# Optimization experiments

Measured on AMD Instinct MI355X. Metric: run time of the kernel, lower is better.

The kernel has to match this reference:

```python
import jax, jax.numpy as jnp
import numpy as np

BETA = 0.9       # neuron_args['beta']
THRESH = 0.5     # neuron_args['threshold'] (mem_thresh)
ALPHA = 2.0      # surrogate.atan(alpha=2)
BIN = 50         # int(0.2 / 0.004)
NSTEPS = 7       # num_steps
STEP = BIN // NSTEPS  # 7 -> only buffer[:49] is used


@jax.custom_vjp
def atan_spike(x):
    return (x > 0).astype(x.dtype)

def _asp_fwd(x):
    return (x > 0).astype(x.dtype), x

def _asp_bwd(x, g):
    return (g * (ALPHA / 2.0) / (1.0 + (jnp.pi / 2.0 * ALPHA * x) ** 2),)

atan_spike.defvjp(_asp_fwd, _asp_bwd)


def _heaviside_detached(x):
    # snntorch mem_reset: reset = spike_grad(mem - thresh).detach()
    return jax.lax.stop_gradient((x > 0).astype(x.dtype))


def _forward(x, W_in, W_h0, W_out, v_x, v_y):
    T, B, D = x.shape
    H = W_in.shape[0]
    O = W_out.shape[0]
    vxy = jnp.concatenate([v_x, v_y])  # (2,)

    def single_forward(acc):  # acc: (NSTEPS, B, D)
        mem1 = jnp.zeros((B, H), x.dtype)
        mem2 = jnp.zeros((B, H), x.dtype)
        mem_out = jnp.zeros((B, O), x.dtype)
        for s in range(NSTEPS):
            cur = acc[s] @ W_in.T                      # (B, H); dropout in eval mode = identity
            reset = _heaviside_detached(mem1 - THRESH)
            mem1 = (BETA * mem1 + cur) * (1.0 - reset)  # reset_mechanism='zero'
            spk = atan_spike(mem1 - THRESH)
            cur = spk @ W_h0.T
            reset = _heaviside_detached(mem2 - THRESH)
            mem2 = (BETA * mem2 + cur) * (1.0 - reset)
            spk = atan_spike(mem2 - THRESH)
            cur = spk @ W_out.T                        # (B, O)
            mem_out = BETA * mem_out + cur             # reset_mechanism='none'
        return mem_out

    def step(carry, x_t):
        buf, L = carry  # buf: (BIN, B, D) zero-padded past L valid frames
        # torch: append then trim front when >BIN. While growing, frames keep
        # fixed positions with zeros at the end (NOT a sliding window yet).
        grow = jax.lax.dynamic_update_slice_in_dim(buf, x_t[None], L, 0)
        slide = jnp.concatenate([buf[1:], x_t[None]], axis=0)
        buf = jnp.where(L < BIN, grow, slide)
        L = jnp.minimum(L + 1, BIN)
        # acc_spikes[i] = sum(buf[7i : 7i+7]); frame 49 unused (49 = 7*7)
        acc = buf[: NSTEPS * STEP].reshape(NSTEPS, STEP, B, D).sum(axis=1)
        pred = single_forward(acc)                     # (B, 2)
        return (buf, L), pred * vxy

    init = (jnp.zeros((BIN, B, D), x.dtype), jnp.int32(1))  # one initial zero frame
    _, preds = jax.lax.scan(step, init, x)             # (T, B, 2)
    return preds


def setup_inputs() -> dict:
    key = jax.random.key(0)
    ks = jax.random.split(key, 6)
    T, B, D, H, O = 128, 1024, 96, 128, 2
    x = jax.random.uniform(ks[0], (T, B, D), dtype=jnp.float32)
    W_in = jax.random.normal(ks[1], (H, D), dtype=jnp.float32) / np.sqrt(D)
    W_h0 = jax.random.normal(ks[2], (H, H), dtype=jnp.float32) / np.sqrt(H)
    W_out = jax.random.normal(ks[3], (O, H), dtype=jnp.float32) / np.sqrt(H)
    v_x = jax.random.normal(ks[4], (1,), dtype=jnp.float32)
    v_y = jax.random.normal(ks[5], (1,), dtype=jnp.float32)
    return {"x": x, "W_in": W_in, "W_h0": W_h0, "W_out": W_out, "v_x": v_x, "v_y": v_y}


def reference(x, W_in, W_h0, W_out, v_x, v_y):
    return _forward(x, W_in, W_h0, W_out, v_x, v_y)
```

## Files before the change

kernel.cpp:

```cpp
#include <hip/hip_runtime.h>
#include <cstdint>

#define T_STEPS 128
#define BATCH   1024
#define D_INPUT 96
#define H_DIM   128
#define NWIN    163

__device__ __forceinline__ void win_decode(int widx, int& start, int& len) {
    if (widx < 121)      { start = widx;        len = 7; }
    else if (widx < 127) { start = 0;           len = widx - 120; }
    else { const int r = widx - 127; const int s = 1 + r / 6;
           len = 1 + r % 6;          start = 7 * s - 1; }
}

__device__ __forceinline__ int widx_for(int t, int s) {
    if (t >= 49) return t - 49 + 7 * s;
    if (s == 0)  return 121 + min(5, t);
    const int st = 7 * s - 1;
    if (t < st) return -1;
    const int len = min(7, t - st + 1);
    return (len == 7) ? st : (127 + (s - 1) * 6 + (len - 1));
}

__device__ __forceinline__ int swz_idx(int row, int col) {
    return (row << 7) | (col ^ ((row & 63) << 1));
}

__global__ __launch_bounds__(256) void kA_wincur(const float* __restrict__ x,
                                                 const float* __restrict__ Win,
                                                 float* __restrict__ CUR1) {
    __shared__ float xs[D_INPUT * 32];
    __shared__ float wT[D_INPUT * H_DIM];
    const int widx = blockIdx.x;
    const int b0   = blockIdx.y * 32;
    int start, len; win_decode(widx, start, len);
    const int tid = threadIdx.x;

    for (int e = tid; e < H_DIM * D_INPUT; e += 256) {
        const int h = e / D_INPUT, d = e % D_INPUT;
        wT[swz_idx(d, h)] = Win[e];
    }
    for (int e = tid; e < D_INPUT * 32; e += 256) {
        const int d = e % D_INPUT, bq = e / D_INPUT;
        const float* xp = x + ((size_t)start * BATCH + b0 + bq) * D_INPUT + d;
        float s = xp[0];
        for (int k = 1; k < len; ++k)
            s = __fadd_rn(s, xp[(size_t)k * BATCH * D_INPUT]);
        xs[d * 32 + bq] = s;
    }
    __syncthreads();

    const int hp = tid & 63, g = tid >> 6;
    const int h0 = hp << 1;
    float acc[8][2];
#pragma unroll
    for (int r = 0; r < 8; ++r) { acc[r][0] = 0.f; acc[r][1] = 0.f; }

#pragma unroll 6
    for (int d = 0; d < D_INPUT; ++d) {
        const float2 wp  = *(const float2*)&wT[swz_idx(d, h0)];
        const float4 xv0 = *(const float4*)&xs[d * 32 + g * 8];
        const float4 xv1 = *(const float4*)&xs[d * 32 + g * 8 + 4];
        const float xv[8] = {xv0.x,xv0.y,xv0.z,xv0.w, xv1.x,xv1.y,xv1.z,xv1.w};
#pragma unroll
        for (int r = 0; r < 8; ++r) {
            acc[r][0] = __fmaf_rn(xv[r], wp.x, acc[r][0]);
            acc[r][1] = __fmaf_rn(xv[r], wp.y, acc[r][1]);
        }
    }
    float* op = CUR1 + ((size_t)widx * BATCH + b0 + g * 8) * H_DIM + h0;
#pragma unroll
    for (int r = 0; r < 8; ++r) {
        float2 o; o.x = acc[r][0]; o.y = acc[r][1];
        *(float2*)(op + (size_t)r * H_DIM) = o;
    }
}

__global__ __launch_bounds__(512, 2) void kB_snn(const float* __restrict__ CUR1,
                                                 const float* __restrict__ Wh0,
                                                 const float* __restrict__ Wout,
                                                 const float* __restrict__ vxp,
                                                 const float* __restrict__ vyp,
                                                 float* __restrict__ out) {
    __shared__ float lw[H_DIM * H_DIM];
    __shared__ float sf[8][64 * 32];
    const int tid = threadIdx.x;
    for (int e = tid; e < H_DIM * H_DIM; e += 512) {
        const int i = e >> 7, h = e & 127;
        lw[swz_idx(h, i)] = Wh0[e];
    }
    __syncthreads();

    const int w = tid >> 6, lane = tid & 63;
    const int t  = blockIdx.y;
    const int i0 = lane << 1;
    float* sfw = sf[w];
    const int lbase = lane * 32;
    const float wex = Wout[i0],     wey = Wout[H_DIM + i0];
    const float wox = Wout[i0 + 1], woy = Wout[H_DIM + i0 + 1];
    const float vx = vxp[0], vy = vyp[0];
    const int b0 = (blockIdx.x << 7) + (w << 4);

    float m1a[16], m1b[16], m2a[16], m2b[16], poa[16], pob[16];
    float c1a[16], c1b[16];
    bool  s1a[16], s1b[16], s2a[16], s2b[16];
#pragma unroll
    for (int k = 0; k < 16; ++k) {
        m1a[k]=0.f; m1b[k]=0.f; m2a[k]=0.f; m2b[k]=0.f; poa[k]=0.f; pob[k]=0.f;
        s1a[k]=false; s1b[k]=false; s2a[k]=false; s2b[k]=false;
    }

    {
        const int wi = widx_for(t, 0);
#pragma unroll
        for (int k = 0; k < 16; ++k) {
            c1a[k] = 0.f; c1b[k] = 0.f;
            if (wi >= 0) {
                const float2 v = *(const float2*)
                    &CUR1[((size_t)wi * BATCH + b0 + k) * H_DIM + i0];
                c1a[k] = v.x; c1b[k] = v.y;
            }
        }
    }

#pragma unroll 1
    for (int s = 0; s < 7; ++s) {
        float sev[16], sov[16];
#pragma unroll
        for (int k = 0; k < 16; ++k) {
            m1a[k] = s1a[k] ? 0.f : __fadd_rn(__fmul_rn(0.9f, m1a[k]), c1a[k]);
            m1b[k] = s1b[k] ? 0.f : __fadd_rn(__fmul_rn(0.9f, m1b[k]), c1b[k]);
            s1a[k] = m1a[k] > 0.5f; s1b[k] = m1b[k] > 0.5f;
            sev[k] = s1a[k] ? 1.0f : 0.0f;
            sov[k] = s1b[k] ? 1.0f : 0.0f;
        }
#pragma unroll
        for (int c = 0; c < 4; ++c) {
            float4 v;
            v.x = sev[c*4]; v.y = sev[c*4+1]; v.z = sev[c*4+2]; v.w = sev[c*4+3];
            *(float4*)&sfw[lbase + ((c     ^ (lane & 7)) << 2)] = v;
            v.x = sov[c*4]; v.y = sov[c*4+1]; v.z = sov[c*4+2]; v.w = sov[c*4+3];
            *(float4*)&sfw[lbase + (((c+4) ^ (lane & 7)) << 2)] = v;
        }

        const int win = (s < 6) ? widx_for(t, s + 1) : -1;
#pragma unroll
        for (int k = 0; k < 16; ++k) {
            c1a[k] = 0.f; c1b[k] = 0.f;
            if (win >= 0) {
                const float2 v = *(const float2*)
                    &CUR1[((size_t)win * BATCH + b0 + k) * H_DIM + i0];
                c1a[k] = v.x; c1b[k] = v.y;
            }
        }

        float c2a[16], c2b[16];
#pragma unroll
        for (int k = 0; k < 16; ++k) { c2a[k] = 0.f; c2b[k] = 0.f; }
#pragma unroll 8
        for (int j = 0; j < 64; ++j) {
            const float2 we = *(const float2*)&lw[swz_idx(2*j,     i0)];
            const float2 wo = *(const float2*)&lw[swz_idx(2*j + 1, i0)];
            const int jb = j * 32, jx = (j & 7) << 2;
            const float4 e0 = *(const float4*)&sfw[jb + ((0  << 2) ^ jx)];
            const float4 e1 = *(const float4*)&sfw[jb + ((1  << 2) ^ jx)];
            const float4 e2 = *(const float4*)&sfw[jb + ((2  << 2) ^ jx)];
            const float4 e3 = *(const float4*)&sfw[jb + ((3  << 2) ^ jx)];
            const float4 o0 = *(const float4*)&sfw[jb + ((4  << 2) ^ jx)];
            const float4 o1 = *(const float4*)&sfw[jb + ((5  << 2) ^ jx)];
            const float4 o2 = *(const float4*)&sfw[jb + ((6  << 2) ^ jx)];
            const float4 o3 = *(const float4*)&sfw[jb + ((7  << 2) ^ jx)];
            const float se[16] = {e0.x,e0.y,e0.z,e0.w, e1.x,e1.y,e1.z,e1.w,
                                  e2.x,e2.y,e2.z,e2.w, e3.x,e3.y,e3.z,e3.w};
            const float so[16] = {o0.x,o0.y,o0.z,o0.w, o1.x,o1.y,o1.z,o1.w,
                                  o2.x,o2.y,o2.z,o2.w, o3.x,o3.y,o3.z,o3.w};
#pragma unroll
            for (int k = 0; k < 16; ++k) {
                c2a[k] = __fmaf_rn(se[k], we.x, c2a[k]);
                c2b[k] = __fmaf_rn(se[k], we.y, c2b[k]);
                c2a[k] = __fmaf_rn(so[k], wo.x, c2a[k]);
                c2b[k] = __fmaf_rn(so[k], wo.y, c2b[k]);
            }
        }

#pragma unroll
        for (int k = 0; k < 16; ++k) {
            m2a[k] = s2a[k] ? 0.f : __fadd_rn(__fmul_rn(0.9f, m2a[k]), c2a[k]);
            m2b[k] = s2b[k] ? 0.f : __fadd_rn(__fmul_rn(0.9f, m2b[k]), c2b[k]);
            s2a[k] = m2a[k] > 0.5f; s2b[k] = m2b[k] > 0.5f;
            const float p0 = (s2a[k] ? wex : 0.f) + (s2b[k] ? wox : 0.f);
            const float p1 = (s2a[k] ? wey : 0.f) + (s2b[k] ? woy : 0.f);
            poa[k] = __fmaf_rn(0.9f, poa[k], p0);
            pob[k] = __fmaf_rn(0.9f, pob[k], p1);
        }
    }

#pragma unroll
    for (int k = 0; k < 16; ++k) {
        float r0 = poa[k], r1 = pob[k];
#pragma unroll
        for (int off = 32; off > 0; off >>= 1) {
            r0 += __shfl_xor(r0, off);
            r1 += __shfl_xor(r1, off);
        }
        if (lane == 0) {
            float2 o;
            o.x = __fmul_rn(r0, vx);
            o.y = __fmul_rn(r1, vy);
            *(float2*)(out + ((size_t)t * BATCH + b0 + k) * 2) = o;
        }
    }
}

extern "C" void kernel_launch(void* const* d_in, const int* in_sizes, int n_in,
                              void* d_out, int out_size, void* d_ws, size_t ws_size,
                              hipStream_t stream) {
    const float* x    = (const float*)d_in[0];
    const float* Win  = (const float*)d_in[1];
    const float* Wh0  = (const float*)d_in[2];
    const float* Wout = (const float*)d_in[3];
    const float* vx   = (const float*)d_in[4];
    const float* vy   = (const float*)d_in[5];
    float* out  = (float*)d_out;
    float* CUR1 = (float*)d_ws;

    kA_wincur<<<dim3(NWIN, BATCH / 32),    dim3(256), 0, stream>>>(x, Win, CUR1);
    kB_snn   <<<dim3(BATCH / 128, T_STEPS), dim3(512), 0, stream>>>(CUR1, Wh0, Wout, vx, vy, out);
}
```

Before: 898.0 us.

## Broadcast activations via readlane instead of LDS staging in both kernels

Both kernels now keep the per-row activation operands in VGPRs and broadcast them to the wavefront with readlane, replacing shared-memory staging. kA loads the summed input window rows into registers. kB drops the spike scratch buffer and its store, and repacks W_h0 into one float4 per (j, lane) so each iteration issues a single LDS read. This removes LDS traffic and shrinks kB's shared-memory footprint, but readlane with a loop-variant lane index needs SGPR moves and scalar-to-vector dependencies that may serialize issue.

```diff
diff --git a/kernel.cpp b/kernel.cpp
--- a/kernel.cpp
+++ b/kernel.cpp
@@ -27,10 +27,14 @@
     return (row << 7) | (col ^ ((row & 63) << 1));
 }
 
+__device__ __forceinline__ float rl_f(float v, int lane) {
+    return __uint_as_float((uint32_t)__builtin_amdgcn_readlane((int)__float_as_uint(v), lane));
+}
+
 __global__ __launch_bounds__(256) void kA_wincur(const float* __restrict__ x,
                                                  const float* __restrict__ Win,
                                                  float* __restrict__ CUR1) {
-    __shared__ float xs[D_INPUT * 32];
+    __shared__ float xs[32 * D_INPUT + 32];
     __shared__ float wT[D_INPUT * H_DIM];
     const int widx = blockIdx.x;
     const int b0   = blockIdx.y * 32;
@@ -41,39 +45,54 @@
         const int h = e / D_INPUT, d = e % D_INPUT;
         wT[swz_idx(d, h)] = Win[e];
     }
-    for (int e = tid; e < D_INPUT * 32; e += 256) {
-        const int d = e % D_INPUT, bq = e / D_INPUT;
+    for (int e = tid; e < 32 * D_INPUT; e += 256) {
+        const int bq = e / D_INPUT, d = e % D_INPUT;
         const float* xp = x + ((size_t)start * BATCH + b0 + bq) * D_INPUT + d;
         float s = xp[0];
         for (int k = 1; k < len; ++k)
             s = __fadd_rn(s, xp[(size_t)k * BATCH * D_INPUT]);
-        xs[d * 32 + bq] = s;
+        xs[bq * D_INPUT + d] = s;
     }
     __syncthreads();
 
-    const int hp = tid & 63, g = tid >> 6;
-    const int h0 = hp << 1;
+    const int lane = tid & 63, g = tid >> 6;
+    const int h0 = lane << 1;
+
+    float wsreg[16];
+#pragma unroll
+    for (int r = 0; r < 16; ++r)
+        wsreg[r] = xs[(8 * (tid >> 6) + (r & 7)) * D_INPUT + ((r >> 3) << 6) + lane];
+
     float acc[8][2];
 #pragma unroll
-    for (int r = 0; r < 8; ++r) { acc[r][0] = 0.f; acc[r][1] = 0.f; }
-
-#pragma unroll 6
-    for (int d = 0; d < D_INPUT; ++d) {
-        const float2 wp  = *(const float2*)&wT[swz_idx(d, h0)];
-        const float4 xv0 = *(const float4*)&xs[d * 32 + g * 8];
-        const float4 xv1 = *(const float4*)&xs[d * 32 + g * 8 + 4];
-        const float xv[8] = {xv0.x,xv0.y,xv0.z,xv0.w, xv1.x,xv1.y,xv1.z,xv1.w};
-#pragma unroll
-        for (int r = 0; r < 8; ++r) {
-            acc[r][0] = __fmaf_rn(xv[r], wp.x, acc[r][0]);
-            acc[r][1] = __fmaf_rn(xv[r], wp.y, acc[r][1]);
-        }
-    }
+    for (int q = 0; q < 8; ++q) { acc[q][0] = 0.f; acc[q][1] = 0.f; }
+
+#pragma unroll 8
+    for (int d = 0; d < 64; ++d) {
+        const float2 wp = *(const float2*)&wT[swz_idx(d, h0)];
+#pragma unroll
+        for (int q = 0; q < 8; ++q) {
+            const float xv = rl_f(wsreg[q], d);
+            acc[q][0] = __fmaf_rn(xv, wp.x, acc[q][0]);
+            acc[q][1] = __fmaf_rn(xv, wp.y, acc[q][1]);
+        }
+    }
+#pragma unroll 8
+    for (int d = 64; d < D_INPUT; ++d) {
+        const float2 wp = *(const float2*)&wT[swz_idx(d, h0)];
+#pragma unroll
+        for (int q = 0; q < 8; ++q) {
+            const float xv = rl_f(wsreg[q + 8], d - 64);
+            acc[q][0] = __fmaf_rn(xv, wp.x, acc[q][0]);
+            acc[q][1] = __fmaf_rn(xv, wp.y, acc[q][1]);
+        }
+    }
+
     float* op = CUR1 + ((size_t)widx * BATCH + b0 + g * 8) * H_DIM + h0;
 #pragma unroll
-    for (int r = 0; r < 8; ++r) {
-        float2 o; o.x = acc[r][0]; o.y = acc[r][1];
-        *(float2*)(op + (size_t)r * H_DIM) = o;
+    for (int q = 0; q < 8; ++q) {
+        float2 o; o.x = acc[q][0]; o.y = acc[q][1];
+        *(float2*)(op + (size_t)q * H_DIM) = o;
     }
 }
 
@@ -83,20 +102,22 @@
                                                  const float* __restrict__ vxp,
                                                  const float* __restrict__ vyp,
                                                  float* __restrict__ out) {
-    __shared__ float lw[H_DIM * H_DIM];
-    __shared__ float sf[8][64 * 32];
+    __shared__ float lwq[64 * 64 * 4];
     const int tid = threadIdx.x;
-    for (int e = tid; e < H_DIM * H_DIM; e += 512) {
-        const int i = e >> 7, h = e & 127;
-        lw[swz_idx(h, i)] = Wh0[e];
+    for (int f = tid; f < 4096; f += 512) {
+        const int j = f >> 6, l = f & 63;
+        float4 v;
+        v.x = Wh0[(2 * l    ) * H_DIM + 2 * j    ];
+        v.y = Wh0[(2 * l + 1) * H_DIM + 2 * j    ];
+        v.z = Wh0[(2 * l    ) * H_DIM + 2 * j + 1];
+        v.w = Wh0[(2 * l + 1) * H_DIM + 2 * j + 1];
+        *(float4*)&lwq[f << 2] = v;
     }
     __syncthreads();
 
     const int w = tid >> 6, lane = tid & 63;
     const int t  = blockIdx.y;
     const int i0 = lane << 1;
-    float* sfw = sf[w];
-    const int lbase = lane * 32;
     const float wex = Wout[i0],     wey = Wout[H_DIM + i0];
     const float wox = Wout[i0 + 1], woy = Wout[H_DIM + i0 + 1];
     const float vx = vxp[0], vy = vyp[0];
@@ -135,14 +156,6 @@
             sev[k] = s1a[k] ? 1.0f : 0.0f;
             sov[k] = s1b[k] ? 1.0f : 0.0f;
         }
-#pragma unroll
-        for (int c = 0; c < 4; ++c) {
-            float4 v;
-            v.x = sev[c*4]; v.y = sev[c*4+1]; v.z = sev[c*4+2]; v.w = sev[c*4+3];
-            *(float4*)&sfw[lbase + ((c     ^ (lane & 7)) << 2)] = v;
-            v.x = sov[c*4]; v.y = sov[c*4+1]; v.z = sov[c*4+2]; v.w = sov[c*4+3];
-            *(float4*)&sfw[lbase + (((c+4) ^ (lane & 7)) << 2)] = v;
-        }
 
         const int win = (s < 6) ? widx_for(t, s + 1) : -1;
 #pragma unroll
@@ -158,29 +171,17 @@
         float c2a[16], c2b[16];
 #pragma unroll
         for (int k = 0; k < 16; ++k) { c2a[k] = 0.f; c2b[k] = 0.f; }
-#pragma unroll 8
+#pragma unroll 4
         for (int j = 0; j < 64; ++j) {
-            const float2 we = *(const float2*)&lw[swz_idx(2*j,     i0)];
-            const float2 wo = *(const float2*)&lw[swz_idx(2*j + 1, i0)];
-            const int jb = j * 32, jx = (j & 7) << 2;
-            const float4 e0 = *(const float4*)&sfw[jb + ((0  << 2) ^ jx)];
-            const float4 e1 = *(const float4*)&sfw[jb + ((1  << 2) ^ jx)];
-            const float4 e2 = *(const float4*)&sfw[jb + ((2  << 2) ^ jx)];
-            const float4 e3 = *(const float4*)&sfw[jb + ((3  << 2) ^ jx)];
-            const float4 o0 = *(const float4*)&sfw[jb + ((4  << 2) ^ jx)];
-            const float4 o1 = *(const float4*)&sfw[jb + ((5  << 2) ^ jx)];
-            const float4 o2 = *(const float4*)&sfw[jb + ((6  << 2) ^ jx)];
-            const float4 o3 = *(const float4*)&sfw[jb + ((7  << 2) ^ jx)];
-            const float se[16] = {e0.x,e0.y,e0.z,e0.w, e1.x,e1.y,e1.z,e1.w,
-                                  e2.x,e2.y,e2.z,e2.w, e3.x,e3.y,e3.z,e3.w};
-            const float so[16] = {o0.x,o0.y,o0.z,o0.w, o1.x,o1.y,o1.z,o1.w,
-                                  o2.x,o2.y,o2.z,o2.w, o3.x,o3.y,o3.z,o3.w};
+            const float4 wq = *(const float4*)&lwq[((j << 6) | lane) << 2];
 #pragma unroll
             for (int k = 0; k < 16; ++k) {
-                c2a[k] = __fmaf_rn(se[k], we.x, c2a[k]);
-                c2b[k] = __fmaf_rn(se[k], we.y, c2b[k]);
-                c2a[k] = __fmaf_rn(so[k], wo.x, c2a[k]);
-                c2b[k] = __fmaf_rn(so[k], wo.y, c2b[k]);
+                const float se = rl_f(sev[k], j);
+                const float so = rl_f(sov[k], j);
+                c2a[k] = __fmaf_rn(se, wq.x, c2a[k]);
+                c2b[k] = __fmaf_rn(se, wq.y, c2b[k]);
+                c2a[k] = __fmaf_rn(so, wq.z, c2a[k]);
+                c2b[k] = __fmaf_rn(so, wq.w, c2b[k]);
             }
         }
 
```

Result: slower. 1.393 ms (+55.1%).
